# Kernel optimization log

Hardware: AMD Instinct MI355X
Metric: run time of the kernel (lower is better)

The kernel has to match this reference:

```python
import jax, jax.numpy as jnp
import numpy as np

TOP_K = 2
NUM_EXPERTS = 8
HIDDEN = 2048
INTER = 1024
TEMP = 1.0


def setup_inputs() -> dict:
    key = jax.random.key(0)
    ks = jax.random.split(key, 5)
    s = 1.0 / np.sqrt(HIDDEN)
    return {
        "hidden_states": jax.random.normal(ks[0], (2, 2048, HIDDEN), jnp.float32),
        "Wr": jax.random.normal(ks[1], (NUM_EXPERTS, HIDDEN), jnp.float32) * s,
        "Wg": jax.random.normal(ks[2], (NUM_EXPERTS, INTER, HIDDEN), jnp.float32) * s,
        "Wu": jax.random.normal(ks[3], (NUM_EXPERTS, INTER, HIDDEN), jnp.float32) * s,
        "Wd": jax.random.normal(ks[4], (NUM_EXPERTS, HIDDEN, INTER), jnp.float32) * (1.0 / np.sqrt(INTER)),
    }


def reference(hidden_states, Wr, Wg, Wu, Wd):
    b, s, d = hidden_states.shape
    x = hidden_states.reshape(-1, d)                      # [t, d]

    # Router: logits over routed experts, top-k, softmax over top-k logits (fp32)
    router_logits = (x @ Wr.T) / TEMP                     # [t, e]
    top_vals, top_idx = jax.lax.top_k(router_logits, TOP_K)  # [t, k]
    routing_weights = jax.nn.softmax(top_vals.astype(jnp.float32), axis=-1).astype(x.dtype)

    # Dense all-expert SwiGLU MLP (equivalent math to per-token dispatch loop)
    g = jnp.einsum('td,efd->tef', x, Wg)                  # [t, e, f]
    u = jnp.einsum('td,efd->tef', x, Wu)
    h = jax.nn.silu(g) * u
    y = jnp.einsum('tef,edf->ted', h, Wd)                 # [t, e, d]

    # Combine: scatter top-k weights into per-expert combine weights
    combine = jnp.zeros((x.shape[0], NUM_EXPERTS), x.dtype)
    combine = combine.at[jnp.arange(x.shape[0])[:, None], top_idx].add(routing_weights)
    out = jnp.einsum('te,ted->td', combine, y)
    return out.reshape(b, s, d), router_logits
```

## Files before the change

### kernel.cpp

```cpp
#include <hip/hip_runtime.h>
#include <hip/hip_bf16.h>

#define NUM_EXPERTS 8
#define HIDDEN 2048
#define INTER 1024
#define NTOK 4096
#define TOPK 2
#define BM 128
#define BK 64
#define MPAD 9216
#define TILES_M 72

typedef __attribute__((ext_vector_type(8))) short bf16x8;
typedef __attribute__((ext_vector_type(4))) float f32x4;

typedef const __attribute__((address_space(1))) unsigned char* gptr_u8;
typedef __attribute__((address_space(3))) unsigned char* lptr_u8;

static __device__ __forceinline__ void gload_lds16(const void* g, void* l) {
    __builtin_amdgcn_global_load_lds((gptr_u8)g, (lptr_u8)l, 16, 0, 0);
}

static __device__ __forceinline__ unsigned short f2bf(float f) {
    unsigned u = __builtin_bit_cast(unsigned, f);
    unsigned rounding = 0x7fffu + ((u >> 16) & 1u);
    u += rounding;
    return (unsigned short)(u >> 16);
}
static __device__ __forceinline__ unsigned pack2(float a, float b) {
    return (unsigned)f2bf(a) | ((unsigned)f2bf(b) << 16);
}

__global__ __launch_bounds__(256) void convert_kernel(
    const float* __restrict__ Wg, const float* __restrict__ Wu,
    const float* __restrict__ Wd, ushort* __restrict__ Wgb,
    ushort* __restrict__ Wub, ushort* __restrict__ Wdb)
{
    const float* src = (blockIdx.y == 0) ? Wg : (blockIdx.y == 1) ? Wu : Wd;
    ushort* dst = (blockIdx.y == 0) ? Wgb : (blockIdx.y == 1) ? Wub : Wdb;
    size_t idx = (size_t)blockIdx.x * 256 + threadIdx.x;
#pragma unroll
    for (int i = 0; i < 4; ++i) {
        size_t p = idx + (size_t)i * 1048576;
        float4 v = ((const float4*)src)[p];
        uint2 u;
        u.x = pack2(v.x, v.y);
        u.y = pack2(v.z, v.w);
        ((uint2*)dst)[p] = u;
    }
}

__global__ __launch_bounds__(256) void router_kernel(
    const float* __restrict__ x, const float* __restrict__ Wr,
    ushort* __restrict__ xbf, float* __restrict__ logits_out,
    int* __restrict__ topk_idx, float* __restrict__ topk_w, int* __restrict__ cnt)
{
    int t = blockIdx.x;
    const float4* xr = (const float4*)(x + (size_t)t * HIDDEN);
    float acc[NUM_EXPERTS];
#pragma unroll
    for (int e = 0; e < NUM_EXPERTS; ++e) acc[e] = 0.f;
#pragma unroll
    for (int i = 0; i < 2; ++i) {
        int d4 = threadIdx.x + i * 256;
        float4 xv = xr[d4];
        if (xbf) {
            uint2 p;
            p.x = pack2(xv.x, xv.y);
            p.y = pack2(xv.z, xv.w);
            *(uint2*)&xbf[(size_t)t * HIDDEN + d4 * 4] = p;
        }
#pragma unroll
        for (int e = 0; e < NUM_EXPERTS; ++e) {
            float4 wv = ((const float4*)(Wr + e * HIDDEN))[d4];
            acc[e] += xv.x * wv.x + xv.y * wv.y + xv.z * wv.z + xv.w * wv.w;
        }
    }
#pragma unroll
    for (int e = 0; e < NUM_EXPERTS; ++e)
        for (int o = 32; o > 0; o >>= 1)
            acc[e] += __shfl_xor(acc[e], o, 64);
    __shared__ float red[4][NUM_EXPERTS];
    int wid = threadIdx.x >> 6, lid = threadIdx.x & 63;
    if (lid == 0) {
#pragma unroll
        for (int e = 0; e < NUM_EXPERTS; ++e) red[wid][e] = acc[e];
    }
    __syncthreads();
    if (threadIdx.x == 0) {
        float l[NUM_EXPERTS];
#pragma unroll
        for (int e = 0; e < NUM_EXPERTS; ++e) {
            l[e] = (red[0][e] + red[1][e] + red[2][e] + red[3][e]);
            logits_out[(size_t)t * NUM_EXPERTS + e] = l[e];
        }
        int i0 = 0; float v0 = l[0];
#pragma unroll
        for (int e = 1; e < NUM_EXPERTS; ++e)
            if (l[e] > v0) { v0 = l[e]; i0 = e; }
        int i1 = -1; float v1 = -1e30f;
#pragma unroll
        for (int e = 0; e < NUM_EXPERTS; ++e) {
            if (e == i0) continue;
            if (i1 < 0 || l[e] > v1) { v1 = l[e]; i1 = e; }
        }
        float e1 = expf(v1 - v0);
        float inv = 1.0f / (1.0f + e1);
        topk_idx[t * 2 + 0] = i0;
        topk_idx[t * 2 + 1] = i1;
        topk_w[t * 2 + 0] = inv;
        topk_w[t * 2 + 1] = e1 * inv;
        atomicAdd(&cnt[i0], 1);
        atomicAdd(&cnt[i1], 1);
    }
}

__global__ __launch_bounds__(256) void setup_kernel(
    const int* __restrict__ cnt, int* __restrict__ cursor,
    int* __restrict__ tile_expert, int* __restrict__ row_token,
    float* __restrict__ row_weight)
{
    if (threadIdx.x == 0) {
        int tot = 0;
        for (int e = 0; e < NUM_EXPERTS; ++e) {
            cursor[e] = tot;
            int pc = ((cnt[e] + BM - 1) / BM) * BM;
            int t0 = tot / BM, t1 = (tot + pc) / BM;
            for (int t = t0; t < t1; ++t) tile_expert[t] = e;
            tot += pc;
        }
        for (int t = tot / BM; t < TILES_M; ++t) tile_expert[t] = 0;
    }
    for (int r = threadIdx.x; r < MPAD; r += 256) {
        row_token[r] = -1;
        row_weight[r] = 0.f;
    }
}

__global__ __launch_bounds__(256) void scatter_kernel(
    const int* __restrict__ topk_idx, const float* __restrict__ topk_w,
    int* __restrict__ cursor, int* __restrict__ row_token,
    float* __restrict__ row_weight)
{
    int t = blockIdx.x * 256 + threadIdx.x;
    if (t >= NTOK) return;
#pragma unroll
    for (int k = 0; k < TOPK; ++k) {
        int e = topk_idx[t * 2 + k];
        float w = topk_w[t * 2 + k];
        int pos = atomicAdd(&cursor[e], 1);
        row_token[pos] = t;
        row_weight[pos] = w;
    }
}

__global__ __launch_bounds__(256) void gemm1_fast(
    const ushort* __restrict__ xbf, const ushort* __restrict__ Wgb,
    const ushort* __restrict__ Wub, const int* __restrict__ row_token,
    const int* __restrict__ tile_expert, ushort* __restrict__ H)
{
    int mtile = blockIdx.x, ntile = blockIdx.y;
    int e = tile_expert[mtile];
    __shared__ __align__(16) ushort As[BM * BK];
    __shared__ __align__(16) ushort Bgs[BM * BK];
    __shared__ __align__(16) ushort Bus[BM * BK];
    int tid = threadIdx.x;
    int rsub = tid >> 3, cc = tid & 7;

    const ushort* aSrc[4];
    const ushort* gSrc[4];
    const ushort* uSrc[4];
#pragma unroll
    for (int it = 0; it < 4; ++it) {
        int r = it * 32 + rsub;
        int tok = row_token[mtile * BM + r];
        if (tok < 0) tok = 0;
        int csw = (cc ^ (r & 7)) * 8;
        aSrc[it] = xbf + (size_t)tok * HIDDEN + csw;
        size_t brow = (size_t)e * INTER + (size_t)ntile * BM + r;
        gSrc[it] = Wgb + brow * HIDDEN + csw;
        uSrc[it] = Wub + brow * HIDDEN + csw;
    }

    f32x4 accG[4][4], accU[4][4];
#pragma unroll
    for (int mi = 0; mi < 4; ++mi)
#pragma unroll
        for (int nj = 0; nj < 4; ++nj) {
            accG[mi][nj] = (f32x4){0.f, 0.f, 0.f, 0.f};
            accU[mi][nj] = (f32x4){0.f, 0.f, 0.f, 0.f};
        }

    int lid = tid & 63, wid = tid >> 6;
    int wm = (wid >> 1) * 64, wn = (wid & 1) * 64;
    int lrow = lid & 15, kg = lid >> 4;

    for (int kk = 0; kk < HIDDEN; kk += BK) {
        __syncthreads();
#pragma unroll
        for (int it = 0; it < 4; ++it) {
            gload_lds16(aSrc[it] + kk, &As[it * 2048 + tid * 8]);
            gload_lds16(gSrc[it] + kk, &Bgs[it * 2048 + tid * 8]);
            gload_lds16(uSrc[it] + kk, &Bus[it * 2048 + tid * 8]);
        }
        __syncthreads();
#pragma unroll
        for (int ks = 0; ks < 2; ++ks) {
            bf16x8 a[4], bg[4], bu[4];
            int kcol = ks * 32 + kg * 8;
#pragma unroll
            for (int mi = 0; mi < 4; ++mi) {
                int r = wm + mi * 16 + lrow;
                a[mi] = *(const bf16x8*)&As[(r * BK + kcol) ^ ((r & 7) << 3)];
            }
#pragma unroll
            for (int nj = 0; nj < 4; ++nj) {
                int r = wn + nj * 16 + lrow;
                int idx = (r * BK + kcol) ^ ((r & 7) << 3);
                bg[nj] = *(const bf16x8*)&Bgs[idx];
                bu[nj] = *(const bf16x8*)&Bus[idx];
            }
#pragma unroll
            for (int mi = 0; mi < 4; ++mi)
#pragma unroll
                for (int nj = 0; nj < 4; ++nj) {
                    accG[mi][nj] = __builtin_amdgcn_mfma_f32_16x16x32_bf16(
                        a[mi], bg[nj], accG[mi][nj], 0, 0, 0);
                    accU[mi][nj] = __builtin_amdgcn_mfma_f32_16x16x32_bf16(
                        a[mi], bu[nj], accU[mi][nj], 0, 0, 0);
                }
        }
    }
#pragma unroll
    for (int mi = 0; mi < 4; ++mi)
#pragma unroll
        for (int nj = 0; nj < 4; ++nj)
#pragma unroll
            for (int q = 0; q < 4; ++q) {
                int row = mtile * BM + wm + mi * 16 + kg * 4 + q;
                int col = ntile * BM + wn + nj * 16 + lrow;
                float g = accG[mi][nj][q], u = accU[mi][nj][q];
                float h = (g / (1.0f + expf(-g))) * u;
                H[(size_t)row * INTER + col] = f2bf(h);
            }
}

__global__ __launch_bounds__(256) void gemm2_fast(
    const ushort* __restrict__ H, const ushort* __restrict__ Wdb,
    const int* __restrict__ row_token, const float* __restrict__ row_weight,
    const int* __restrict__ tile_expert, float* __restrict__ out)
{
    int mtile = blockIdx.x, ntile = blockIdx.y;
    int e = tile_expert[mtile];
    __shared__ __align__(16) ushort As[BM * BK];
    __shared__ __align__(16) ushort Bs[BM * BK];
    __shared__ int s_tok[BM];
    __shared__ float s_w[BM];
    int tid = threadIdx.x;
    if (tid < BM) {
        s_tok[tid] = row_token[mtile * BM + tid];
        s_w[tid] = row_weight[mtile * BM + tid];
    }
    int rsub = tid >> 3, cc = tid & 7;

    const ushort* aSrc[4];
    const ushort* bSrc[4];
#pragma unroll
    for (int it = 0; it < 4; ++it) {
        int r = it * 32 + rsub;
        int csw = (cc ^ (r & 7)) * 8;
        aSrc[it] = H + (size_t)(mtile * BM + r) * INTER + csw;
        size_t brow = (size_t)e * HIDDEN + (size_t)ntile * BM + r;
        bSrc[it] = Wdb + brow * INTER + csw;
    }

    f32x4 acc[4][4];
#pragma unroll
    for (int mi = 0; mi < 4; ++mi)
#pragma unroll
        for (int nj = 0; nj < 4; ++nj)
            acc[mi][nj] = (f32x4){0.f, 0.f, 0.f, 0.f};

    int lid = tid & 63, wid = tid >> 6;
    int wm = (wid >> 1) * 64, wn = (wid & 1) * 64;
    int lrow = lid & 15, kg = lid >> 4;

    for (int kk = 0; kk < INTER; kk += BK) {
        __syncthreads();
#pragma unroll
        for (int it = 0; it < 4; ++it) {
            gload_lds16(aSrc[it] + kk, &As[it * 2048 + tid * 8]);
            gload_lds16(bSrc[it] + kk, &Bs[it * 2048 + tid * 8]);
        }
        __syncthreads();
#pragma unroll
        for (int ks = 0; ks < 2; ++ks) {
            bf16x8 a[4], b[4];
            int kcol = ks * 32 + kg * 8;
#pragma unroll
            for (int mi = 0; mi < 4; ++mi) {
                int r = wm + mi * 16 + lrow;
                a[mi] = *(const bf16x8*)&As[(r * BK + kcol) ^ ((r & 7) << 3)];
            }
#pragma unroll
            for (int nj = 0; nj < 4; ++nj) {
                int r = wn + nj * 16 + lrow;
                b[nj] = *(const bf16x8*)&Bs[(r * BK + kcol) ^ ((r & 7) << 3)];
            }
#pragma unroll
            for (int mi = 0; mi < 4; ++mi)
#pragma unroll
                for (int nj = 0; nj < 4; ++nj)
                    acc[mi][nj] = __builtin_amdgcn_mfma_f32_16x16x32_bf16(
                        a[mi], b[nj], acc[mi][nj], 0, 0, 0);
        }
    }
#pragma unroll
    for (int mi = 0; mi < 4; ++mi)
#pragma unroll
        for (int nj = 0; nj < 4; ++nj)
#pragma unroll
            for (int q = 0; q < 4; ++q) {
                int lrow_local = wm + mi * 16 + kg * 4 + q;
                int tok = s_tok[lrow_local];
                if (tok >= 0) {
                    int col = ntile * BM + wn + nj * 16 + lrow;
                    float val = acc[mi][nj][q] * s_w[lrow_local];
                    atomicAdd(&out[(size_t)tok * HIDDEN + col], val);
                }
            }
}

__global__ __launch_bounds__(256) void gemm1_slow(
    const float* __restrict__ x, const float* __restrict__ Wg,
    const float* __restrict__ Wu, const int* __restrict__ row_token,
    const int* __restrict__ tile_expert, ushort* __restrict__ H)
{
    int mtile = blockIdx.x, ntile = blockIdx.y;
    int e = tile_expert[mtile];
    __shared__ ushort As[BM * BK];
    __shared__ ushort Bgs[BM * BK];
    __shared__ ushort Bus[BM * BK];
    __shared__ int s_tok[BM];
    int tid = threadIdx.x;
    if (tid < BM) s_tok[tid] = row_token[mtile * BM + tid];

    const float* WgB = Wg + (size_t)e * INTER * HIDDEN + (size_t)(ntile * BM) * HIDDEN;
    const float* WuB = Wu + (size_t)e * INTER * HIDDEN + (size_t)(ntile * BM) * HIDDEN;

    f32x4 accG[4][4], accU[4][4];
#pragma unroll
    for (int mi = 0; mi < 4; ++mi)
#pragma unroll
        for (int nj = 0; nj < 4; ++nj) {
            accG[mi][nj] = (f32x4){0.f, 0.f, 0.f, 0.f};
            accU[mi][nj] = (f32x4){0.f, 0.f, 0.f, 0.f};
        }

    int lid = tid & 63, wid = tid >> 6;
    int wm = (wid >> 1) * 64, wn = (wid & 1) * 64;
    int lrow = lid & 15, kg = lid >> 4;

    for (int kk = 0; kk < HIDDEN; kk += BK) {
        __syncthreads();
#pragma unroll
        for (int it = 0; it < 8; ++it) {
            int i = it * 256 + tid;
            int r = i >> 4, c = (i & 15) * 4;
            int tok = s_tok[r];
            float4 v = make_float4(0.f, 0.f, 0.f, 0.f);
            if (tok >= 0)
                v = *(const float4*)(x + (size_t)tok * HIDDEN + kk + c);
            uint2 p;
            p.x = pack2(v.x, v.y);
            p.y = pack2(v.z, v.w);
            int idx = (r * BK + c) ^ ((r & 7) << 3);
            *(uint2*)&As[idx] = p;
        }
#pragma unroll
        for (int it = 0; it < 8; ++it) {
            int i = it * 256 + tid;
            int r = i >> 4, c = (i & 15) * 4;
            float4 vg = *(const float4*)(WgB + (size_t)r * HIDDEN + kk + c);
            float4 vu = *(const float4*)(WuB + (size_t)r * HIDDEN + kk + c);
            int idx = (r * BK + c) ^ ((r & 7) << 3);
            uint2 pg, pu;
            pg.x = pack2(vg.x, vg.y);
            pg.y = pack2(vg.z, vg.w);
            pu.x = pack2(vu.x, vu.y);
            pu.y = pack2(vu.z, vu.w);
            *(uint2*)&Bgs[idx] = pg;
            *(uint2*)&Bus[idx] = pu;
        }
        __syncthreads();
#pragma unroll
        for (int ks = 0; ks < 2; ++ks) {
            bf16x8 a[4], bg[4], bu[4];
            int kcol = ks * 32 + kg * 8;
#pragma unroll
            for (int mi = 0; mi < 4; ++mi) {
                int r = wm + mi * 16 + lrow;
                a[mi] = *(const bf16x8*)&As[(r * BK + kcol) ^ ((r & 7) << 3)];
            }
#pragma unroll
            for (int nj = 0; nj < 4; ++nj) {
                int r = wn + nj * 16 + lrow;
                int idx = (r * BK + kcol) ^ ((r & 7) << 3);
                bg[nj] = *(const bf16x8*)&Bgs[idx];
                bu[nj] = *(const bf16x8*)&Bus[idx];
            }
#pragma unroll
            for (int mi = 0; mi < 4; ++mi)
#pragma unroll
                for (int nj = 0; nj < 4; ++nj) {
                    accG[mi][nj] = __builtin_amdgcn_mfma_f32_16x16x32_bf16(
                        a[mi], bg[nj], accG[mi][nj], 0, 0, 0);
                    accU[mi][nj] = __builtin_amdgcn_mfma_f32_16x16x32_bf16(
                        a[mi], bu[nj], accU[mi][nj], 0, 0, 0);
                }
        }
    }
#pragma unroll
    for (int mi = 0; mi < 4; ++mi)
#pragma unroll
        for (int nj = 0; nj < 4; ++nj)
#pragma unroll
            for (int q = 0; q < 4; ++q) {
                int row = mtile * BM + wm + mi * 16 + kg * 4 + q;
                int col = ntile * BM + wn + nj * 16 + lrow;
                float g = accG[mi][nj][q], u = accU[mi][nj][q];
                float h = (g / (1.0f + expf(-g))) * u;
                H[(size_t)row * INTER + col] = f2bf(h);
            }
}

__global__ __launch_bounds__(256) void gemm2_slow(
    const ushort* __restrict__ H, const float* __restrict__ Wd,
    const int* __restrict__ row_token, const float* __restrict__ row_weight,
    const int* __restrict__ tile_expert, float* __restrict__ out)
{
    int mtile = blockIdx.x, ntile = blockIdx.y;
    int e = tile_expert[mtile];
    __shared__ ushort As[BM * BK];
    __shared__ ushort Bs[BM * BK];
    __shared__ int s_tok[BM];
    __shared__ float s_w[BM];
    int tid = threadIdx.x;
    if (tid < BM) {
        s_tok[tid] = row_token[mtile * BM + tid];
        s_w[tid] = row_weight[mtile * BM + tid];
    }

    const float* WdB = Wd + (size_t)e * HIDDEN * INTER + (size_t)(ntile * BM) * INTER;

    f32x4 acc[4][4];
#pragma unroll
    for (int mi = 0; mi < 4; ++mi)
#pragma unroll
        for (int nj = 0; nj < 4; ++nj)
            acc[mi][nj] = (f32x4){0.f, 0.f, 0.f, 0.f};

    int lid = tid & 63, wid = tid >> 6;
    int wm = (wid >> 1) * 64, wn = (wid & 1) * 64;
    int lrow = lid & 15, kg = lid >> 4;

    for (int kk = 0; kk < INTER; kk += BK) {
        __syncthreads();
#pragma unroll
        for (int it = 0; it < 4; ++it) {
            int i = it * 256 + tid;
            int r = i >> 3, c = (i & 7) * 8;
            uint4 v = *(const uint4*)(H + (size_t)(mtile * BM + r) * INTER + kk + c);
            int idx = (r * BK + c) ^ ((r & 7) << 3);
            *(uint4*)&As[idx] = v;
        }
#pragma unroll
        for (int it = 0; it < 8; ++it) {
            int i = it * 256 + tid;
            int r = i >> 4, c = (i & 15) * 4;
            float4 v = *(const float4*)(WdB + (size_t)r * INTER + kk + c);
            int idx = (r * BK + c) ^ ((r & 7) << 3);
            uint2 p;
            p.x = pack2(v.x, v.y);
            p.y = pack2(v.z, v.w);
            *(uint2*)&Bs[idx] = p;
        }
        __syncthreads();
#pragma unroll
        for (int ks = 0; ks < 2; ++ks) {
            bf16x8 a[4], b[4];
            int kcol = ks * 32 + kg * 8;
#pragma unroll
            for (int mi = 0; mi < 4; ++mi) {
                int r = wm + mi * 16 + lrow;
                a[mi] = *(const bf16x8*)&As[(r * BK + kcol) ^ ((r & 7) << 3)];
            }
#pragma unroll
            for (int nj = 0; nj < 4; ++nj) {
                int r = wn + nj * 16 + lrow;
                b[nj] = *(const bf16x8*)&Bs[(r * BK + kcol) ^ ((r & 7) << 3)];
            }
#pragma unroll
            for (int mi = 0; mi < 4; ++mi)
#pragma unroll
                for (int nj = 0; nj < 4; ++nj)
                    acc[mi][nj] = __builtin_amdgcn_mfma_f32_16x16x32_bf16(
                        a[mi], b[nj], acc[mi][nj], 0, 0, 0);
        }
    }
#pragma unroll
    for (int mi = 0; mi < 4; ++mi)
#pragma unroll
        for (int nj = 0; nj < 4; ++nj)
#pragma unroll
            for (int q = 0; q < 4; ++q) {
                int lrow_local = wm + mi * 16 + kg * 4 + q;
                int tok = s_tok[lrow_local];
                if (tok >= 0) {
                    int col = ntile * BM + wn + nj * 16 + lrow;
                    float val = acc[mi][nj][q] * s_w[lrow_local];
                    atomicAdd(&out[(size_t)tok * HIDDEN + col], val);
                }
            }
}

extern "C" void kernel_launch(void* const* d_in, const int* in_sizes, int n_in,
                              void* d_out, int out_size, void* d_ws, size_t ws_size,
                              hipStream_t stream) {
    const float* x  = (const float*)d_in[0];
    const float* Wr = (const float*)d_in[1];
    const float* Wg = (const float*)d_in[2];
    const float* Wu = (const float*)d_in[3];
    const float* Wd = (const float*)d_in[4];
    float* out = (float*)d_out;
    float* logits = out + (size_t)NTOK * HIDDEN;

    char* ws = (char*)d_ws;
    int*    cnt         = (int*)(ws + 0);
    int*    cursor      = (int*)(ws + 64);
    int*    tile_expert = (int*)(ws + 128);
    int*    topk_idx    = (int*)(ws + 512);
    float*  topk_w      = (float*)(ws + 33280);
    int*    row_token   = (int*)(ws + 66048);
    float*  row_weight  = (float*)(ws + 102912);

    const size_t FAST_NEED = 136462336ull;
    bool fast = ws_size >= FAST_NEED;

    hipMemsetAsync(d_out, 0, (size_t)out_size * sizeof(float), stream);
    hipMemsetAsync(d_ws, 0, 128, stream);

    if (fast) {
        ushort* xbf = (ushort*)(ws + 147456);
        ushort* H   = (ushort*)(ws + 16924672);
        ushort* Wgb = (ushort*)(ws + 35799040);
        ushort* Wub = (ushort*)(ws + 69353472);
        ushort* Wdb = (ushort*)(ws + 102907904);

        convert_kernel<<<dim3(4096, 3), 256, 0, stream>>>(Wg, Wu, Wd, Wgb, Wub, Wdb);
        router_kernel<<<NTOK, 256, 0, stream>>>(x, Wr, xbf, logits, topk_idx, topk_w, cnt);
        setup_kernel<<<1, 256, 0, stream>>>(cnt, cursor, tile_expert, row_token, row_weight);
        scatter_kernel<<<NTOK / 256, 256, 0, stream>>>(topk_idx, topk_w, cursor, row_token, row_weight);
        gemm1_fast<<<dim3(TILES_M, INTER / BM), 256, 0, stream>>>(xbf, Wgb, Wub, row_token, tile_expert, H);
        gemm2_fast<<<dim3(TILES_M, HIDDEN / BM), 256, 0, stream>>>(H, Wdb, row_token, row_weight, tile_expert, out);
    } else {
        ushort* H = (ushort*)(ws + 147456);
        router_kernel<<<NTOK, 256, 0, stream>>>(x, Wr, (ushort*)nullptr, logits, topk_idx, topk_w, cnt);
        setup_kernel<<<1, 256, 0, stream>>>(cnt, cursor, tile_expert, row_token, row_weight);
        scatter_kernel<<<NTOK / 256, 256, 0, stream>>>(topk_idx, topk_w, cursor, row_token, row_weight);
        gemm1_slow<<<dim3(TILES_M, INTER / BM), 256, 0, stream>>>(x, Wg, Wu, row_token, tile_expert, H);
        gemm2_slow<<<dim3(TILES_M, HIDDEN / BM), 256, 0, stream>>>(H, Wd, row_token, row_weight, tile_expert, out);
    }
}
```

Before: 676.2 us.

## Replace atomic expert combine with bf16 Y buffer and gather-combine kernel

The down-projection GEMM now writes each routed row's result as bf16 into a padded Y buffer instead of weighting it and atomically adding it into the fp32 output. A new per-token combine kernel gathers the token's two rows, applies the routing weights and writes the output directly, so the output memset is no longer needed on the fast path. The scatter kernel records each token's row position in topk_idx for this gather. In addition, gemm1 tiles shrink to 64 columns in N to launch more blocks, and both GEMMs use a swizzled 1D block order for L2 locality. The trade-offs are an extra bf16 rounding of the per-expert outputs and one more kernel launch plus a Y round-trip through memory.

```diff
diff --git a/kernel.cpp b/kernel.cpp
--- a/kernel.cpp
+++ b/kernel.cpp
@@ -30,6 +30,9 @@
 static __device__ __forceinline__ unsigned pack2(float a, float b) {
     return (unsigned)f2bf(a) | ((unsigned)f2bf(b) << 16);
 }
+static __device__ __forceinline__ float bf2f(unsigned short u) {
+    return __builtin_bit_cast(float, ((unsigned)u) << 16);
+}
 
 __global__ __launch_bounds__(256) void convert_kernel(
     const float* __restrict__ Wg, const float* __restrict__ Wu,
@@ -138,19 +141,20 @@
 }
 
 __global__ __launch_bounds__(256) void scatter_kernel(
-    const int* __restrict__ topk_idx, const float* __restrict__ topk_w,
+    const int* __restrict__ topk_idx_in, const float* __restrict__ topk_w,
     int* __restrict__ cursor, int* __restrict__ row_token,
-    float* __restrict__ row_weight)
+    float* __restrict__ row_weight, int* __restrict__ topk_idx_out)
 {
     int t = blockIdx.x * 256 + threadIdx.x;
     if (t >= NTOK) return;
 #pragma unroll
     for (int k = 0; k < TOPK; ++k) {
-        int e = topk_idx[t * 2 + k];
+        int e = topk_idx_in[t * 2 + k] & 15;
         float w = topk_w[t * 2 + k];
         int pos = atomicAdd(&cursor[e], 1);
         row_token[pos] = t;
         row_weight[pos] = w;
+        topk_idx_out[t * 2 + k] = (pos << 4) | e;
     }
 }
 
@@ -159,17 +163,19 @@
     const ushort* __restrict__ Wub, const int* __restrict__ row_token,
     const int* __restrict__ tile_expert, ushort* __restrict__ H)
 {
-    int mtile = blockIdx.x, ntile = blockIdx.y;
+    int bid = blockIdx.x;
+    int swz = (bid & 7) * 144 + (bid >> 3);
+    int mtile = swz >> 4, ntile = swz & 15;
     int e = tile_expert[mtile];
     __shared__ __align__(16) ushort As[BM * BK];
-    __shared__ __align__(16) ushort Bgs[BM * BK];
-    __shared__ __align__(16) ushort Bus[BM * BK];
+    __shared__ __align__(16) ushort Bgs[64 * BK];
+    __shared__ __align__(16) ushort Bus[64 * BK];
     int tid = threadIdx.x;
     int rsub = tid >> 3, cc = tid & 7;
 
     const ushort* aSrc[4];
-    const ushort* gSrc[4];
-    const ushort* uSrc[4];
+    const ushort* gSrc[2];
+    const ushort* uSrc[2];
 #pragma unroll
     for (int it = 0; it < 4; ++it) {
         int r = it * 32 + rsub;
@@ -177,36 +183,43 @@
         if (tok < 0) tok = 0;
         int csw = (cc ^ (r & 7)) * 8;
         aSrc[it] = xbf + (size_t)tok * HIDDEN + csw;
-        size_t brow = (size_t)e * INTER + (size_t)ntile * BM + r;
+    }
+#pragma unroll
+    for (int it = 0; it < 2; ++it) {
+        int r = it * 32 + rsub;
+        int csw = (cc ^ (r & 7)) * 8;
+        size_t brow = (size_t)e * INTER + (size_t)ntile * 64 + r;
         gSrc[it] = Wgb + brow * HIDDEN + csw;
         uSrc[it] = Wub + brow * HIDDEN + csw;
     }
 
-    f32x4 accG[4][4], accU[4][4];
-#pragma unroll
-    for (int mi = 0; mi < 4; ++mi)
-#pragma unroll
-        for (int nj = 0; nj < 4; ++nj) {
+    f32x4 accG[4][2], accU[4][2];
+#pragma unroll
+    for (int mi = 0; mi < 4; ++mi)
+#pragma unroll
+        for (int nj = 0; nj < 2; ++nj) {
             accG[mi][nj] = (f32x4){0.f, 0.f, 0.f, 0.f};
             accU[mi][nj] = (f32x4){0.f, 0.f, 0.f, 0.f};
         }
 
     int lid = tid & 63, wid = tid >> 6;
-    int wm = (wid >> 1) * 64, wn = (wid & 1) * 64;
+    int wm = (wid >> 1) * 64, wn = (wid & 1) * 32;
     int lrow = lid & 15, kg = lid >> 4;
 
     for (int kk = 0; kk < HIDDEN; kk += BK) {
         __syncthreads();
 #pragma unroll
-        for (int it = 0; it < 4; ++it) {
+        for (int it = 0; it < 4; ++it)
             gload_lds16(aSrc[it] + kk, &As[it * 2048 + tid * 8]);
+#pragma unroll
+        for (int it = 0; it < 2; ++it) {
             gload_lds16(gSrc[it] + kk, &Bgs[it * 2048 + tid * 8]);
             gload_lds16(uSrc[it] + kk, &Bus[it * 2048 + tid * 8]);
         }
         __syncthreads();
 #pragma unroll
         for (int ks = 0; ks < 2; ++ks) {
-            bf16x8 a[4], bg[4], bu[4];
+            bf16x8 a[4], bg[2], bu[2];
             int kcol = ks * 32 + kg * 8;
 #pragma unroll
             for (int mi = 0; mi < 4; ++mi) {
@@ -214,7 +227,7 @@
                 a[mi] = *(const bf16x8*)&As[(r * BK + kcol) ^ ((r & 7) << 3)];
             }
 #pragma unroll
-            for (int nj = 0; nj < 4; ++nj) {
+            for (int nj = 0; nj < 2; ++nj) {
                 int r = wn + nj * 16 + lrow;
                 int idx = (r * BK + kcol) ^ ((r & 7) << 3);
                 bg[nj] = *(const bf16x8*)&Bgs[idx];
@@ -223,7 +236,7 @@
 #pragma unroll
             for (int mi = 0; mi < 4; ++mi)
 #pragma unroll
-                for (int nj = 0; nj < 4; ++nj) {
+                for (int nj = 0; nj < 2; ++nj) {
                     accG[mi][nj] = __builtin_amdgcn_mfma_f32_16x16x32_bf16(
                         a[mi], bg[nj], accG[mi][nj], 0, 0, 0);
                     accU[mi][nj] = __builtin_amdgcn_mfma_f32_16x16x32_bf16(
@@ -234,11 +247,11 @@
 #pragma unroll
     for (int mi = 0; mi < 4; ++mi)
 #pragma unroll
-        for (int nj = 0; nj < 4; ++nj)
+        for (int nj = 0; nj < 2; ++nj)
 #pragma unroll
             for (int q = 0; q < 4; ++q) {
                 int row = mtile * BM + wm + mi * 16 + kg * 4 + q;
-                int col = ntile * BM + wn + nj * 16 + lrow;
+                int col = ntile * 64 + wn + nj * 16 + lrow;
                 float g = accG[mi][nj][q], u = accU[mi][nj][q];
                 float h = (g / (1.0f + expf(-g))) * u;
                 H[(size_t)row * INTER + col] = f2bf(h);
@@ -247,20 +260,15 @@
 
 __global__ __launch_bounds__(256) void gemm2_fast(
     const ushort* __restrict__ H, const ushort* __restrict__ Wdb,
-    const int* __restrict__ row_token, const float* __restrict__ row_weight,
-    const int* __restrict__ tile_expert, float* __restrict__ out)
-{
-    int mtile = blockIdx.x, ntile = blockIdx.y;
+    const int* __restrict__ tile_expert, ushort* __restrict__ Y)
+{
+    int bid = blockIdx.x;
+    int swz = (bid & 7) * 144 + (bid >> 3);
+    int mtile = swz >> 4, ntile = swz & 15;
     int e = tile_expert[mtile];
     __shared__ __align__(16) ushort As[BM * BK];
     __shared__ __align__(16) ushort Bs[BM * BK];
-    __shared__ int s_tok[BM];
-    __shared__ float s_w[BM];
     int tid = threadIdx.x;
-    if (tid < BM) {
-        s_tok[tid] = row_token[mtile * BM + tid];
-        s_w[tid] = row_weight[mtile * BM + tid];
-    }
     int rsub = tid >> 3, cc = tid & 7;
 
     const ushort* aSrc[4];
@@ -321,14 +329,35 @@
         for (int nj = 0; nj < 4; ++nj)
 #pragma unroll
             for (int q = 0; q < 4; ++q) {
-                int lrow_local = wm + mi * 16 + kg * 4 + q;
-                int tok = s_tok[lrow_local];
-                if (tok >= 0) {
-                    int col = ntile * BM + wn + nj * 16 + lrow;
-                    float val = acc[mi][nj][q] * s_w[lrow_local];
-                    atomicAdd(&out[(size_t)tok * HIDDEN + col], val);
-                }
-            }
+                int row = mtile * BM + wm + mi * 16 + kg * 4 + q;
+                int col = ntile * BM + wn + nj * 16 + lrow;
+                Y[(size_t)row * HIDDEN + col] = f2bf(acc[mi][nj][q]);
+            }
+}
+
+__global__ __launch_bounds__(256) void combine_kernel(
+    const ushort* __restrict__ Y, const int* __restrict__ topk_idx,
+    const float* __restrict__ topk_w, float* __restrict__ out)
+{
+    int t = blockIdx.x;
+    int r0 = topk_idx[t * 2 + 0] >> 4;
+    int r1 = topk_idx[t * 2 + 1] >> 4;
+    float w0 = topk_w[t * 2 + 0];
+    float w1 = topk_w[t * 2 + 1];
+    int c = threadIdx.x * 8;
+    uint4 y0 = *(const uint4*)&Y[(size_t)r0 * HIDDEN + c];
+    uint4 y1 = *(const uint4*)&Y[(size_t)r1 * HIDDEN + c];
+    float o[8];
+    const unsigned* p0 = (const unsigned*)&y0;
+    const unsigned* p1 = (const unsigned*)&y1;
+#pragma unroll
+    for (int i = 0; i < 4; ++i) {
+        o[i * 2]     = w0 * bf2f((ushort)(p0[i] & 0xffff)) + w1 * bf2f((ushort)(p1[i] & 0xffff));
+        o[i * 2 + 1] = w0 * bf2f((ushort)(p0[i] >> 16))    + w1 * bf2f((ushort)(p1[i] >> 16));
+    }
+    float4* dst = (float4*)&out[(size_t)t * HIDDEN + c];
+    dst[0] = make_float4(o[0], o[1], o[2], o[3]);
+    dst[1] = make_float4(o[4], o[5], o[6], o[7]);
 }
 
 __global__ __launch_bounds__(256) void gemm1_slow(
@@ -547,27 +576,29 @@
     const size_t FAST_NEED = 136462336ull;
     bool fast = ws_size >= FAST_NEED;
 
-    hipMemsetAsync(d_out, 0, (size_t)out_size * sizeof(float), stream);
     hipMemsetAsync(d_ws, 0, 128, stream);
 
     if (fast) {
         ushort* xbf = (ushort*)(ws + 147456);
-        ushort* H   = (ushort*)(ws + 16924672);
-        ushort* Wgb = (ushort*)(ws + 35799040);
-        ushort* Wub = (ushort*)(ws + 69353472);
+        ushort* Wgb = (ushort*)(ws + 16924672);
+        ushort* Wub = (ushort*)(ws + 50479104);
+        ushort* H   = (ushort*)(ws + 84033536);
         ushort* Wdb = (ushort*)(ws + 102907904);
+        ushort* Y   = (ushort*)(ws + 147456);
 
         convert_kernel<<<dim3(4096, 3), 256, 0, stream>>>(Wg, Wu, Wd, Wgb, Wub, Wdb);
         router_kernel<<<NTOK, 256, 0, stream>>>(x, Wr, xbf, logits, topk_idx, topk_w, cnt);
         setup_kernel<<<1, 256, 0, stream>>>(cnt, cursor, tile_expert, row_token, row_weight);
-        scatter_kernel<<<NTOK / 256, 256, 0, stream>>>(topk_idx, topk_w, cursor, row_token, row_weight);
-        gemm1_fast<<<dim3(TILES_M, INTER / BM), 256, 0, stream>>>(xbf, Wgb, Wub, row_token, tile_expert, H);
-        gemm2_fast<<<dim3(TILES_M, HIDDEN / BM), 256, 0, stream>>>(H, Wdb, row_token, row_weight, tile_expert, out);
+        scatter_kernel<<<NTOK / 256, 256, 0, stream>>>(topk_idx, topk_w, cursor, row_token, row_weight, topk_idx);
+        gemm1_fast<<<TILES_M * 16, 256, 0, stream>>>(xbf, Wgb, Wub, row_token, tile_expert, H);
+        gemm2_fast<<<TILES_M * 16, 256, 0, stream>>>(H, Wdb, tile_expert, Y);
+        combine_kernel<<<NTOK, 256, 0, stream>>>(Y, topk_idx, topk_w, out);
     } else {
         ushort* H = (ushort*)(ws + 147456);
+        hipMemsetAsync(d_out, 0, (size_t)out_size * sizeof(float), stream);
         router_kernel<<<NTOK, 256, 0, stream>>>(x, Wr, (ushort*)nullptr, logits, topk_idx, topk_w, cnt);
         setup_kernel<<<1, 256, 0, stream>>>(cnt, cursor, tile_expert, row_token, row_weight);
-        scatter_kernel<<<NTOK / 256, 256, 0, stream>>>(topk_idx, topk_w, cursor, row_token, row_weight);
+        scatter_kernel<<<NTOK / 256, 256, 0, stream>>>(topk_idx, topk_w, cursor, row_token, row_weight, topk_idx);
         gemm1_slow<<<dim3(TILES_M, INTER / BM), 256, 0, stream>>>(x, Wg, Wu, row_token, tile_expert, H);
         gemm2_slow<<<dim3(TILES_M, HIDDEN / BM), 256, 0, stream>>>(H, Wd, row_token, row_weight, tile_expert, out);
     }
```

After: 559.4 us. -17.3%, faster.
